# Performance work log

Measured on AMD Instinct MI355X. Metric: run time of the kernel, lower is better.

The kernel has to match this reference:

```python
import jax, jax.numpy as jnp
import numpy as np

EMBED_DIM = 768


def setup_inputs() -> dict:
    key = jax.random.key(0)
    k1, k2, k3, k4, k5 = jax.random.split(key, 5)
    C = EMBED_DIM
    B, N = 32, 1024
    s = 1.0 / np.sqrt(C)
    x = jax.random.normal(k1, (B, N, C), dtype=jnp.float32)
    qkv_w = jax.random.normal(k2, (C, 3 * C), dtype=jnp.float32) * s  # [in, out]
    qkv_b = jax.random.normal(k3, (3 * C,), dtype=jnp.float32) * 0.02
    proj_w = jax.random.normal(k4, (C, C), dtype=jnp.float32) * s
    proj_b = jax.random.normal(k5, (C,), dtype=jnp.float32) * 0.02
    return {"x": x, "qkv_w": qkv_w, "qkv_b": qkv_b, "proj_w": proj_w, "proj_b": proj_b}


def reference(x, qkv_w, qkv_b, proj_w, proj_b):
    B, N, C = x.shape
    qkv = (x @ qkv_w + qkv_b).reshape(B, N, 3, C)
    q, k, v = qkv[:, :, 0], qkv[:, :, 1], qkv[:, :, 2]  # each [B, N, C]
    # single-head full attention; scale by sqrt(C) as in source
    scores = jnp.einsum('bnc,bmc->bnm', q, k) / jnp.sqrt(jnp.asarray(C, x.dtype))
    attn = jax.nn.softmax(scores, axis=-1)  # dropout p=0.0 -> identity
    out = jnp.einsum('bnm,bmc->bnc', attn, v)
    # faithful to source: transpose(1,2).reshape(B,N,C) permutes the data
    out = jnp.swapaxes(out, 1, 2).reshape(B, N, C)
    return out @ proj_w + proj_b
```

## Files before the change

### kernel.cpp

```cpp
#include <hip/hip_runtime.h>
#include <hip/hip_bf16.h>


#define BM 256
#define BN 256
#define BKK 64

typedef __attribute__((ext_vector_type(8))) short bf16x8;
typedef __attribute__((ext_vector_type(4))) float f32x4;

__device__ __forceinline__ unsigned short f2b(float f) {
  unsigned int u = __float_as_uint(f);
  u = u + 0x7fffu + ((u >> 16) & 1u);
  return (unsigned short)(u >> 16);
}

__device__ __forceinline__ void g2l16(const void* g, void* l) {
  __builtin_amdgcn_global_load_lds(
      (const __attribute__((address_space(1))) unsigned int*)g,
      (__attribute__((address_space(3))) unsigned int*)l, 16, 0, 0);
}

template <int EPI>
__global__ __launch_bounds__(512, 2) void gemm_nt8(
    const unsigned short* __restrict__ A, const unsigned short* __restrict__ B,
    unsigned short* __restrict__ Cb, unsigned short* __restrict__ Ck,
    unsigned short* __restrict__ Cv, float* __restrict__ Cf,
    const float* __restrict__ bias, float* __restrict__ Z, int K, int lda,
    int ldb, int ldc, long bsA, long bsB, long bsC, float scale, int MT,
    int NN) {
  __shared__ unsigned short As[2][2][BM][32];
  __shared__ unsigned short Bs[2][2][BN][32];

  const int id = blockIdx.x;
  const int w = (id & 7) * ((int)gridDim.x >> 3) + (id >> 3);
  const int pb = MT * NN;
  const int bz = w / pb;
  const int r = w - bz * pb;
  const int bym = r / NN;
  const int bxn = r - bym * NN;

  const unsigned short* Ag = A + (long)bz * bsA + (long)(bym * BM) * lda;
  const unsigned short* Bg = B + (long)bz * bsB + (long)(bxn * BN) * ldb;

  const int tid = threadIdx.x;
  const int wave = tid >> 6;
  const int lane = tid & 63;
  const int l15 = lane & 15;
  const int lk = lane >> 4;
  const int wm = (wave >> 2) << 7;
  const int wn = (wave & 3) << 6;

  const int sr = lane >> 2;
  const int scq = (lane & 3) ^ (sr & 3);

  f32x4 acc[8][4];
#pragma unroll
  for (int m = 0; m < 8; ++m)
#pragma unroll
    for (int n = 0; n < 4; ++n)
#pragma unroll
      for (int p = 0; p < 4; ++p) acc[m][n][p] = 0.f;

  auto stA = [&](int b, int s, int k0) {
#pragma unroll
    for (int i = 0; i < 2; ++i) {
      const int rb = (wave << 5) + (i << 4);
      g2l16(Ag + (long)(rb + sr) * lda + k0 + (s << 5) + (scq << 3),
            &As[b][s][rb][0]);
    }
  };
  auto stB = [&](int b, int s, int k0) {
#pragma unroll
    for (int i = 0; i < 2; ++i) {
      const int rb = (wave << 5) + (i << 4);
      g2l16(Bg + (long)(rb + sr) * ldb + k0 + (s << 5) + (scq << 3),
            &Bs[b][s][rb][0]);
    }
  };
  auto ldA = [&](int b, int s, int m) {
    return *(const bf16x8*)&As[b][s][wm + (m << 4) + l15]
                              [((lk ^ (l15 & 3)) << 3)];
  };
  auto ldB = [&](int b, int s, int n) {
    return *(const bf16x8*)&Bs[b][s][wn + (n << 4) + l15]
                              [((lk ^ (l15 & 3)) << 3)];
  };

  const int NT = K / BKK;
  const int NIT = NT >> 1;

  stA(0, 0, 0); stA(0, 1, 0); stB(0, 0, 0); stB(0, 1, 0);
  stB(1, 0, BKK); stA(1, 0, BKK); stB(1, 1, BKK);
  asm volatile("s_waitcnt vmcnt(6)" ::: "memory");
  __builtin_amdgcn_sched_barrier(0);
  __builtin_amdgcn_s_barrier();
  __builtin_amdgcn_sched_barrier(0);

  bf16x8 bf[4], af[4];

#define PHASE(b, s, mh, RDB, STAGE_STMT, VM_STMT)                          \
  {                                                                        \
    if (RDB) {                                                             \
      _Pragma("unroll") for (int n = 0; n < 4; ++n) bf[n] = ldB(b, s, n);  \
    }                                                                      \
    _Pragma("unroll") for (int m = 0; m < 4; ++m) af[m] =                  \
        ldA(b, s, (mh << 2) + m);                                          \
    STAGE_STMT;                                                            \
    __builtin_amdgcn_sched_barrier(0);                                     \
    __builtin_amdgcn_s_barrier();                                          \
    asm volatile("s_waitcnt lgkmcnt(0)" ::: "memory");                     \
    __builtin_amdgcn_sched_barrier(0);                                     \
    __builtin_amdgcn_s_setprio(1);                                         \
    _Pragma("unroll") for (int m = 0; m < 4; ++m)                          \
      _Pragma("unroll") for (int n = 0; n < 4; ++n)                        \
        acc[(mh << 2) + m][n] = __builtin_amdgcn_mfma_f32_16x16x32_bf16(   \
            af[m], bf[n], acc[(mh << 2) + m][n], 0, 0, 0);                 \
    __builtin_amdgcn_s_setprio(0);                                         \
    VM_STMT;                                                               \
    __builtin_amdgcn_s_barrier();                                          \
  }

  for (int k = 0; k < NIT; ++k) {
    const bool g = (k + 1 < NIT);
    const int kt1 = (2 * k + 1) * BKK;
    const int ku0 = (2 * k + 2) * BKK;
    const int ku1 = (2 * k + 3) * BKK;

    PHASE(0, 0, 0, true, { stA(1, 1, kt1); }, {});
    PHASE(0, 0, 1, false, { if (g) stB(0, 0, ku0); }, {});
    PHASE(0, 1, 0, true, { if (g) stA(0, 0, ku0); }, {});
    PHASE(0, 1, 1, false, { if (g) stB(0, 1, ku0); }, {
      if (g)
        asm volatile("s_waitcnt vmcnt(6)" ::: "memory");
      else
        asm volatile("s_waitcnt vmcnt(0)" ::: "memory");
      __builtin_amdgcn_sched_barrier(0);
    });
    PHASE(1, 0, 0, true, { if (g) stA(0, 1, ku0); }, {});
    PHASE(1, 0, 1, false, { if (g) stB(1, 0, ku1); }, {});
    PHASE(1, 1, 0, true, { if (g) stA(1, 0, ku1); }, {});
    PHASE(1, 1, 1, false, { if (g) stB(1, 1, ku1); }, {
      if (g) {
        asm volatile("s_waitcnt vmcnt(6)" ::: "memory");
        __builtin_amdgcn_sched_barrier(0);
      }
    });
  }
#undef PHASE

  const int row0 = bym * BM + wm + (lk << 2);
  const int col0 = bxn * BN + wn;

  if constexpr (EPI == 1) {
    const int seg = (bxn * BN) / 768;
    unsigned short* O = (seg == 0) ? Cb : ((seg == 1) ? Ck : Cv);
    float bv2[4];
#pragma unroll
    for (int n = 0; n < 4; ++n) bv2[n] = bias[col0 + (n << 4) + l15];
    const int cl0 = col0 + l15 - seg * 768;
#pragma unroll
    for (int m = 0; m < 8; ++m)
#pragma unroll
      for (int p = 0; p < 4; ++p) {
        const long rr = row0 + (m << 4) + p;
#pragma unroll
        for (int n = 0; n < 4; ++n)
          O[rr * 768 + cl0 + (n << 4)] = f2b(acc[m][n][p] + bv2[n]);
      }
  } else if constexpr (EPI == 2) {
    float bv2[4];
#pragma unroll
    for (int n = 0; n < 4; ++n) bv2[n] = bias[col0 + (n << 4) + l15];
#pragma unroll
    for (int m = 0; m < 8; ++m)
#pragma unroll
      for (int p = 0; p < 4; ++p) {
        const long rr = row0 + (m << 4) + p;
#pragma unroll
        for (int n = 0; n < 4; ++n)
          Cf[rr * ldc + col0 + (n << 4) + l15] = acc[m][n][p] + bv2[n];
      }
  } else if constexpr (EPI == 3) {
    unsigned short* C = Cb + (long)bz * bsC;
#pragma unroll
    for (int m = 0; m < 8; ++m) {
      float es[4] = {0.f, 0.f, 0.f, 0.f};
#pragma unroll
      for (int p = 0; p < 4; ++p) {
        const long rr = row0 + (m << 4) + p;
#pragma unroll
        for (int n = 0; n < 4; ++n) {
          const float e = __expf(acc[m][n][p] * scale);
          es[p] += e;
          C[rr * ldc + col0 + (n << 4) + l15] = f2b(e);
        }
      }
#pragma unroll
      for (int p = 0; p < 4; ++p) {
        float s = es[p];
        s += __shfl_xor(s, 1);
        s += __shfl_xor(s, 2);
        s += __shfl_xor(s, 4);
        s += __shfl_xor(s, 8);
        if (l15 == 0)
          atomicAdd(&Z[(long)bz * 1024 + row0 + (m << 4) + p], s);
      }
    }
  } else {
    unsigned short* C = Cb + (long)bz * bsC;
    float zv[4];
#pragma unroll
    for (int n = 0; n < 4; ++n)
      zv[n] = 1.f / Z[(long)bz * 1024 + col0 + (n << 4) + l15];
#pragma unroll
    for (int m = 0; m < 8; ++m)
#pragma unroll
      for (int p = 0; p < 4; ++p) {
        const long rr = row0 + (m << 4) + p;
#pragma unroll
        for (int n = 0; n < 4; ++n)
          C[rr * ldc + col0 + (n << 4) + l15] = f2b(acc[m][n][p] * zv[n]);
      }
  }
}

__global__ __launch_bounds__(256) void prep(
    const float4* __restrict__ x, ushort4* __restrict__ x_bf,
    const float* __restrict__ qkv_w, unsigned short* __restrict__ Wqkv,
    const float* __restrict__ proj_w, unsigned short* __restrict__ Wp) {
  const int blk = blockIdx.x;
  if (blk < 24576) {
    const long i = (long)blk * 256 + threadIdx.x;
    float4 f = x[i];
    ushort4 o;
    o.x = f2b(f.x); o.y = f2b(f.y); o.z = f2b(f.z); o.w = f2b(f.w);
    x_bf[i] = o;
  } else if (blk < 24576 + 6912) {
    const long i = (long)(blk - 24576) * 256 + threadIdx.x;
    const int k = (int)(i % 768);
    const int j = (int)(i / 768);
    Wqkv[i] = f2b(qkv_w[(long)k * 2304 + j]);
  } else {
    const long i = (long)(blk - 24576 - 6912) * 256 + threadIdx.x;
    const int k = (int)(i % 768);
    const int j = (int)(i / 768);
    Wp[i] = f2b(proj_w[(long)k * 768 + j]);
  }
}

__global__ __launch_bounds__(256) void transpose_v(
    const unsigned short* __restrict__ V, unsigned short* __restrict__ Vt) {
  __shared__ unsigned short T[64][72];
  const int b = blockIdx.z;
  const int d0 = blockIdx.x << 6;
  const int m0 = blockIdx.y << 6;
  const unsigned short* Vb = V + (long)b * 786432;
  unsigned short* Vtb = Vt + (long)b * 786432;
  const int tid = threadIdx.x;
  const int r = tid >> 2;
  const int c4 = tid & 3;
#pragma unroll
  for (int h = 0; h < 2; ++h) {
    const int cc = (c4 + (h << 2)) << 3;
    *(uint4*)&T[r][cc] = *(const uint4*)&Vb[(long)(m0 + r) * 768 + d0 + cc];
  }
  __syncthreads();
#pragma unroll
  for (int h = 0; h < 2; ++h) {
    const int mm = (c4 + (h << 2)) << 3;
    alignas(16) unsigned short tmp[8];
#pragma unroll
    for (int e = 0; e < 8; ++e) tmp[e] = T[mm + e][r];
    *(uint4*)&Vtb[(long)(d0 + r) * 1024 + m0 + mm] = *(uint4*)tmp;
  }
}

extern "C" void kernel_launch(void* const* d_in, const int* in_sizes, int n_in,
                              void* d_out, int out_size, void* d_ws,
                              size_t ws_size, hipStream_t stream) {
  const float* x = (const float*)d_in[0];
  const float* qkv_w = (const float*)d_in[1];
  const float* qkv_b = (const float*)d_in[2];
  const float* proj_w = (const float*)d_in[3];
  const float* proj_b = (const float*)d_in[4];
  float* out = (float*)d_out;

  char* ws = (char*)d_ws;
  unsigned short* x_bf = (unsigned short*)ws;
  unsigned short* Wqkv = (unsigned short*)(ws + 50331648);
  unsigned short* Wp = (unsigned short*)(ws + 53870592);
  unsigned short* Qb = (unsigned short*)(ws + 55050240);
  unsigned short* Kb = (unsigned short*)(ws + 105381888);
  unsigned short* Vb = (unsigned short*)(ws + 155713536);
  unsigned short* Sb = (unsigned short*)(ws + 206045184);
  unsigned short* Vt = x_bf;
  unsigned short* Hb = Qb;
  float* Zs = (float*)Vb;

  prep<<<33792, 256, 0, stream>>>((const float4*)x, (ushort4*)x_bf, qkv_w,
                                  Wqkv, proj_w, Wp);

  gemm_nt8<1><<<1152, 512, 0, stream>>>(
      x_bf, Wqkv, Qb, Kb, Vb, nullptr, qkv_b, nullptr, 768, 768, 768, 0, 0, 0,
      0, 1.f, 128, 9);

  transpose_v<<<dim3(12, 16, 32), 256, 0, stream>>>(Vb, Vt);

  hipMemsetAsync(Zs, 0, 32 * 1024 * sizeof(float), stream);

  gemm_nt8<3><<<512, 512, 0, stream>>>(
      Qb, Kb, Sb, nullptr, nullptr, nullptr, nullptr, Zs, 768, 768, 768, 1024,
      786432, 786432, 1048576, 0.03608439182435161f, 4, 4);

  gemm_nt8<4><<<384, 512, 0, stream>>>(
      Vt, Sb, Hb, nullptr, nullptr, nullptr, nullptr, Zs, 1024, 1024, 1024,
      1024, 786432, 1048576, 786432, 1.f, 3, 4);

  gemm_nt8<2><<<384, 512, 0, stream>>>(
      Hb, Wp, nullptr, nullptr, nullptr, out, proj_b, nullptr, 768, 768, 768,
      768, 0, 0, 0, 1.f, 128, 3);
}
```

Measured before the change: 568.0 us.

## Restructure LDS tiles to full 64-wide K rows with 8-way XOR swizzle

The shared-memory tiles change from two 32-column K halves to a single 64-column row per tile, with an 8-chunk XOR swizzle on both the global-to-LDS stores and the fragment reads. Each staging lane now writes 8 lanes per row instead of 4, giving longer contiguous global segments per row. The prefetch schedule is reorganised so each stage load covers both row halves in one phase, with fewer issue points and adjusted vmcnt waits. The aim is better global coalescing and fewer LDS bank conflicts. The trade-off is burstier load issue and less even spreading of loads across the compute phases.

```diff
diff --git a/kernel.cpp b/kernel.cpp
--- a/kernel.cpp
+++ b/kernel.cpp
@@ -29,8 +29,8 @@
     const float* __restrict__ bias, float* __restrict__ Z, int K, int lda,
     int ldb, int ldc, long bsA, long bsB, long bsC, float scale, int MT,
     int NN) {
-  __shared__ unsigned short As[2][2][BM][32];
-  __shared__ unsigned short Bs[2][2][BN][32];
+  __shared__ unsigned short As[2][BM][BKK];
+  __shared__ unsigned short Bs[2][BN][BKK];
 
   const int id = blockIdx.x;
   const int w = (id & 7) * ((int)gridDim.x >> 3) + (id >> 3);
@@ -51,8 +51,8 @@
   const int wm = (wave >> 2) << 7;
   const int wn = (wave & 3) << 6;
 
-  const int sr = lane >> 2;
-  const int scq = (lane & 3) ^ (sr & 3);
+  const int sr = lane >> 3;
+  const int sc = (lane & 7) ^ sr;
 
   f32x4 acc[8][4];
 #pragma unroll
@@ -62,50 +62,48 @@
 #pragma unroll
       for (int p = 0; p < 4; ++p) acc[m][n][p] = 0.f;
 
-  auto stA = [&](int b, int s, int k0) {
+  auto stA = [&](int d, int h, int k0) {
 #pragma unroll
     for (int i = 0; i < 2; ++i) {
-      const int rb = (wave << 5) + (i << 4);
-      g2l16(Ag + (long)(rb + sr) * lda + k0 + (s << 5) + (scq << 3),
-            &As[b][s][rb][0]);
+      const int rb = (h << 7) + (wave << 4) + (i << 3);
+      g2l16(Ag + (long)(rb + sr) * lda + k0 + (sc << 3), &As[d][rb][0]);
     }
   };
-  auto stB = [&](int b, int s, int k0) {
+  auto stB = [&](int d, int h, int k0) {
 #pragma unroll
     for (int i = 0; i < 2; ++i) {
-      const int rb = (wave << 5) + (i << 4);
-      g2l16(Bg + (long)(rb + sr) * ldb + k0 + (s << 5) + (scq << 3),
-            &Bs[b][s][rb][0]);
+      const int rb = (h << 7) + (wave << 4) + (i << 3);
+      g2l16(Bg + (long)(rb + sr) * ldb + k0 + (sc << 3), &Bs[d][rb][0]);
     }
   };
-  auto ldA = [&](int b, int s, int m) {
-    return *(const bf16x8*)&As[b][s][wm + (m << 4) + l15]
-                              [((lk ^ (l15 & 3)) << 3)];
+  auto ldA = [&](int d, int m, int ks) {
+    return *(const bf16x8*)&As[d][wm + (m << 4) + l15]
+                              [((((ks << 2) | lk) ^ (l15 & 7)) << 3)];
   };
-  auto ldB = [&](int b, int s, int n) {
-    return *(const bf16x8*)&Bs[b][s][wn + (n << 4) + l15]
-                              [((lk ^ (l15 & 3)) << 3)];
+  auto ldB = [&](int d, int n, int ks) {
+    return *(const bf16x8*)&Bs[d][wn + (n << 4) + l15]
+                              [((((ks << 2) | lk) ^ (l15 & 7)) << 3)];
   };
 
   const int NT = K / BKK;
   const int NIT = NT >> 1;
 
   stA(0, 0, 0); stA(0, 1, 0); stB(0, 0, 0); stB(0, 1, 0);
-  stB(1, 0, BKK); stA(1, 0, BKK); stB(1, 1, BKK);
-  asm volatile("s_waitcnt vmcnt(6)" ::: "memory");
+  stB(1, 0, BKK); stB(1, 1, BKK);
+  asm volatile("s_waitcnt vmcnt(4)" ::: "memory");
   __builtin_amdgcn_sched_barrier(0);
   __builtin_amdgcn_s_barrier();
   __builtin_amdgcn_sched_barrier(0);
 
   bf16x8 bf[4], af[4];
 
-#define PHASE(b, s, mh, RDB, STAGE_STMT, VM_STMT)                          \
+#define PHASE(b, ks, mh, RDB, STAGE_STMT, VM_STMT)                         \
   {                                                                        \
     if (RDB) {                                                             \
-      _Pragma("unroll") for (int n = 0; n < 4; ++n) bf[n] = ldB(b, s, n);  \
+      _Pragma("unroll") for (int n = 0; n < 4; ++n) bf[n] = ldB(b, n, ks); \
     }                                                                      \
     _Pragma("unroll") for (int m = 0; m < 4; ++m) af[m] =                  \
-        ldA(b, s, (mh << 2) + m);                                          \
+        ldA(b, (mh << 2) + m, ks);                                         \
     STAGE_STMT;                                                            \
     __builtin_amdgcn_sched_barrier(0);                                     \
     __builtin_amdgcn_s_barrier();                                          \
@@ -127,22 +125,22 @@
     const int ku0 = (2 * k + 2) * BKK;
     const int ku1 = (2 * k + 3) * BKK;
 
-    PHASE(0, 0, 0, true, { stA(1, 1, kt1); }, {});
-    PHASE(0, 0, 1, false, { if (g) stB(0, 0, ku0); }, {});
-    PHASE(0, 1, 0, true, { if (g) stA(0, 0, ku0); }, {});
-    PHASE(0, 1, 1, false, { if (g) stB(0, 1, ku0); }, {
+    PHASE(0, 0, 0, true, { stA(1, 0, kt1); stA(1, 1, kt1); }, {});
+    PHASE(0, 0, 1, false, {}, {});
+    PHASE(0, 1, 0, true, {}, {});
+    PHASE(0, 1, 1, false, { if (g) { stB(0, 0, ku0); stB(0, 1, ku0); } }, {
       if (g)
-        asm volatile("s_waitcnt vmcnt(6)" ::: "memory");
+        asm volatile("s_waitcnt vmcnt(4)" ::: "memory");
       else
         asm volatile("s_waitcnt vmcnt(0)" ::: "memory");
       __builtin_amdgcn_sched_barrier(0);
     });
-    PHASE(1, 0, 0, true, { if (g) stA(0, 1, ku0); }, {});
-    PHASE(1, 0, 1, false, { if (g) stB(1, 0, ku1); }, {});
-    PHASE(1, 1, 0, true, { if (g) stA(1, 0, ku1); }, {});
-    PHASE(1, 1, 1, false, { if (g) stB(1, 1, ku1); }, {
+    PHASE(1, 0, 0, true, { if (g) { stA(0, 0, ku0); stA(0, 1, ku0); } }, {});
+    PHASE(1, 0, 1, false, {}, {});
+    PHASE(1, 1, 0, true, {}, {});
+    PHASE(1, 1, 1, false, { if (g) { stB(1, 0, ku1); stB(1, 1, ku1); } }, {
       if (g) {
-        asm volatile("s_waitcnt vmcnt(6)" ::: "memory");
+        asm volatile("s_waitcnt vmcnt(4)" ::: "memory");
         __builtin_amdgcn_sched_barrier(0);
       }
     });
```

Result: slower. 654.0 us (+15.2%).
